# Optimization experiments

Measured on AMD Instinct MI355X. Metric: run time of the kernel, lower is better.

Reference implementation:

```python
import jax, jax.numpy as jnp
import numpy as np

EMBED_DIM = 1024
NUM_HEADS = 16
HEAD_DIM = EMBED_DIM // NUM_HEADS  # 64
GROUP_SIZE = 4                     # 4 values packed per uint8 (2-bit KIVI)
Q_LEVELS = 3.0                     # 2-bit -> codes in [0, 3]
Q_HALF = 1.5                       # symmetric offset


def kivi_fake_quant(k):
    """Per-group 2-bit quantize+dequantize of keys, KIVI-style.
    k: [B, H, S, D] float32. Groups of GROUP_SIZE along D share one fp32 scale
    (mirrors k_cache_packed uint8 codes + k_scales fp32 in the source).
    """
    B, H, S, D = k.shape
    g = k.reshape(B, H, S, D // GROUP_SIZE, GROUP_SIZE)
    max_abs = jnp.max(jnp.abs(g), axis=-1, keepdims=True)        # per-group scale basis
    scale = max_abs / Q_HALF
    safe = jnp.where(scale == 0, 1.0, scale)
    codes = jnp.clip(jnp.round(g / safe + Q_HALF), 0.0, Q_LEVELS)  # uint8 codes (as float)
    deq = (codes - Q_HALF) * scale                                 # dequant
    return deq.reshape(B, H, S, D)


def split_heads(x):
    B, S, E = x.shape
    return x.reshape(B, S, NUM_HEADS, HEAD_DIM).transpose(0, 2, 1, 3)  # [B,H,S,d]


def setup_inputs() -> dict:
    key = jax.random.key(0)
    k1, k2, k3 = jax.random.split(key, 3)
    B, S = 4, 1024
    return {
        "hidden_states": jax.random.normal(k1, (B, S, EMBED_DIM), jnp.float32),
        "attention_mask": jnp.zeros((B, S), jnp.float32),  # additive mask
        "w_attn": jax.random.normal(k2, (EMBED_DIM, 3 * EMBED_DIM), jnp.float32) * 0.02,
        "b_attn": jnp.zeros((3 * EMBED_DIM,), jnp.float32),
        "w_proj": jax.random.normal(k3, (EMBED_DIM, EMBED_DIM), jnp.float32) * 0.02,
        "b_proj": jnp.zeros((EMBED_DIM,), jnp.float32),
    }


def reference(hidden_states, attention_mask, w_attn, b_attn, w_proj, b_proj):
    B, S, E = hidden_states.shape
    qkv = hidden_states @ w_attn + b_attn            # GPT-2 Conv1D: x @ W + b
    q, k, v = jnp.split(qkv, 3, axis=2)
    q, k, v = split_heads(q), split_heads(k), split_heads(v)   # [B,H,S,d]

    k_deq = kivi_fake_quant(k)                       # quantized KV cache (keys)
    # kivi_sycl.batched_attention: q @ dequant(K)^T over full cache_len (== S here)
    scores = jnp.einsum('bhqd,bhkd->bhqk', q, k_deq)
    # source adds 2-D additive mask BEFORE the 1/sqrt(d) scaling
    scores = scores + attention_mask[:, None, None, :]
    attn = jax.nn.softmax(scores / jnp.sqrt(jnp.float32(HEAD_DIM)), axis=-1)

    out = jnp.einsum('bhqk,bhkd->bhqd', attn, v)     # V cache kept fp32
    out = out.transpose(0, 2, 1, 3).reshape(B, S, E)
    return out @ w_proj + b_proj
```

## Files before the change

### kernel.cpp

```cpp
#include <hip/hip_runtime.h>
#include <math.h>

#define S_LEN 1024
#define B_SZ  4
#define E_DIM 1024
#define NH    16
#define HD    64
#define GK    1024

typedef unsigned short u16;
typedef _Float16 f16;
typedef __attribute__((ext_vector_type(8))) _Float16 f16x8;
typedef __attribute__((ext_vector_type(2))) __fp16   hf16x2;
typedef __attribute__((ext_vector_type(4))) float    f32x4;

#define MFMA16(a, b, c) __builtin_amdgcn_mfma_f32_16x16x32_f16(a, b, c, 0, 0, 0)
#define SCALE2 0.18033688011112042f

__device__ __forceinline__ u16 f2h_bits(float f) {
    union { f16 h; u16 u; } c; c.h = (f16)f;
    return c.u;
}
__device__ __forceinline__ unsigned pk2h(float a, float b) {
    return (unsigned)f2h_bits(a) | ((unsigned)f2h_bits(b) << 16);
}
__device__ __forceinline__ unsigned pkrtz2(float a, float b) {
    hf16x2 t = __builtin_amdgcn_cvt_pkrtz(a, b);
    union { hf16x2 v; unsigned u; } c; c.v = t; return c.u;
}

__device__ __forceinline__ void glds16(const u16* g, u16* l) {
    __builtin_amdgcn_global_load_lds(
        (const __attribute__((address_space(1))) unsigned int*)g,
        (__attribute__((address_space(3))) unsigned int*)l, 16, 0, 0);
}

__global__ __launch_bounds__(256) void prep_all(
    const float* __restrict__ hs, u16* __restrict__ Hh,
    const float* __restrict__ w_attn, u16* __restrict__ Wqt,
    const float* __restrict__ w_proj, u16* __restrict__ Wpt,
    const float* __restrict__ mask, float* __restrict__ Msc)
{
    __shared__ float t[32][33];
    const int bid = blockIdx.x;

    if (bid == 8192) {
        const int i = threadIdx.x * 16;
        #pragma unroll
        for (int k = 0; k < 4; ++k) {
            float4 v = *(const float4*)&mask[i + 4 * k];
            float4 o = { v.x * SCALE2, v.y * SCALE2, v.z * SCALE2, v.w * SCALE2 };
            *(float4*)&Msc[i + 4 * k] = o;
        }
        return;
    }
    if (bid < 4096) {
        const size_t i = ((size_t)bid * 256 + threadIdx.x) * 4;
        float4 v = *(const float4*)&hs[i];
        ushort4 h;
        h.x = f2h_bits(v.x); h.y = f2h_bits(v.y);
        h.z = f2h_bits(v.z); h.w = f2h_bits(v.w);
        *(ushort4*)&Hh[i] = h;
        return;
    }

    const bool isA = bid < 7168;
    const int tt = isA ? (bid - 4096) : (bid - 7168);
    const int bxx = isA ? (tt % 96) : (tt % 32);
    const int byy = isA ? (tt / 96) : (tt / 32);
    const int N   = isA ? 3072 : 1024;
    const float* W = isA ? w_attn : w_proj;
    u16* Wt = isA ? Wqt : Wpt;

    const int k0 = byy * 32, n0 = bxx * 32;
    {
        const int kr = threadIdx.x >> 3, nc = (threadIdx.x & 7) << 2;
        float4 v = *(const float4*)&W[(size_t)(k0 + kr) * N + n0 + nc];
        t[kr][nc] = v.x; t[kr][nc + 1] = v.y; t[kr][nc + 2] = v.z; t[kr][nc + 3] = v.w;
    }
    __syncthreads();
    const int nr = threadIdx.x >> 3, kc = (threadIdx.x & 7) << 2;
    ushort4 h;
    h.x = f2h_bits(t[kc + 0][nr]); h.y = f2h_bits(t[kc + 1][nr]);
    h.z = f2h_bits(t[kc + 2][nr]); h.w = f2h_bits(t[kc + 3][nr]);
    *(ushort4*)&Wt[(size_t)(n0 + nr) * GK + k0 + kc] = h;
}

__global__ __launch_bounds__(256, 3) void qkv_gemm(
    const u16* __restrict__ A, const u16* __restrict__ Bt,
    const float* __restrict__ bias, u16* __restrict__ Qh,
    u16* __restrict__ Kh, u16* __restrict__ Vtg)
{
    __shared__ u16 SLDS[16896];
    u16* Asp = SLDS;
    u16* Bsp = SLDS + 8192;

    const int tid = threadIdx.x;
    const int wave = tid >> 6, lane = tid & 63;
    const int quad = lane >> 4, l15 = lane & 15;
    const int wr = wave >> 1, wc = wave & 1;

    const int m0   = blockIdx.y * 128;
    const int nloc = blockIdx.x * 128;
    const int region = nloc >> 10;

    const u16* Ab = A  + (size_t)m0 * GK;
    const u16* Bb = Bt + (size_t)nloc * GK;

    const int soff = (((lane & 7) ^ ((lane >> 3) & 7)) << 3);
    const int srow8 = lane >> 3;
    const int sw = l15 & 7;

    f32x4 acc[4][4] = {};

    for (int k0 = 0; k0 < GK; k0 += 64) {
        __syncthreads();
        #pragma unroll
        for (int i = 0; i < 4; ++i) {
            const int tI = wave * 4 + i;
            const int row = tI * 8 + srow8;
            glds16(Ab + (size_t)row * GK + k0 + soff, &Asp[tI * 512]);
            glds16(Bb + (size_t)row * GK + k0 + soff, &Bsp[tI * 512]);
        }
        __syncthreads();
        #pragma unroll
        for (int h = 0; h < 2; ++h) {
            const int cs = ((4 * h + quad) ^ sw) << 3;
            f16x8 af[4], bf[4];
            #pragma unroll
            for (int i = 0; i < 4; ++i)
                af[i] = *(const f16x8*)&Asp[(64 * wr + 16 * i + l15) * 64 + cs];
            #pragma unroll
            for (int j = 0; j < 4; ++j)
                bf[j] = *(const f16x8*)&Bsp[(64 * wc + 16 * j + l15) * 64 + cs];
            #pragma unroll
            for (int i = 0; i < 4; ++i)
                #pragma unroll
                for (int j = 0; j < 4; ++j)
                    acc[i][j] = MFMA16(af[i], bf[j], acc[i][j]);
        }
    }

    if (region == 2) {
        #pragma unroll
        for (int j = 0; j < 4; ++j) {
            const int colg = nloc + 64 * wc + 16 * j + l15;
            const float bv = bias[colg];
            const int cr = colg & 1023, h = cr >> 6, d = cr & 63;
            #pragma unroll
            for (int i = 0; i < 4; ++i) {
                const int rowb = m0 + 64 * wr + 16 * i + quad * 4;
                const int b = rowb >> 10, s0 = rowb & 1023;
                float v0 = acc[i][j][0] + bv, v1 = acc[i][j][1] + bv;
                float v2 = acc[i][j][2] + bv, v3 = acc[i][j][3] + bv;
                uint2 st = { pk2h(v0, v1), pk2h(v2, v3) };
                *(uint2*)&Vtg[((size_t)(b * NH + h) * HD + d) * S_LEN + s0] = st;
            }
        }
    } else {
        float* EP = (float*)SLDS;
        u16* dstg = (region == 1) ? Kh : Qh;
        #pragma unroll
        for (int p = 0; p < 2; ++p) {
            __syncthreads();
            if (wr == p) {
                #pragma unroll
                for (int i = 0; i < 4; ++i)
                    #pragma unroll
                    for (int j = 0; j < 4; ++j) {
                        const int colb = 64 * wc + 16 * j + l15;
                        const float bv = bias[nloc + colb];
                        #pragma unroll
                        for (int r = 0; r < 4; ++r)
                            EP[(16 * i + quad * 4 + r) * 132 + colb] = acc[i][j][r] + bv;
                    }
            }
            __syncthreads();
            const int rr = tid >> 2, cc = (tid & 3) * 32;
            const int rowg = m0 + 64 * p + rr;
            const int bb = rowg >> 10, ss = rowg & 1023;
            float v[32];
            #pragma unroll
            for (int k = 0; k < 8; ++k) {
                f32x4 t4 = *(const f32x4*)&EP[rr * 132 + cc + 4 * k];
                v[4 * k + 0] = t4[0]; v[4 * k + 1] = t4[1];
                v[4 * k + 2] = t4[2]; v[4 * k + 3] = t4[3];
            }
            if (region == 1) {
                #pragma unroll
                for (int g = 0; g < 8; ++g) {
                    float a = fmaxf(fmaxf(fabsf(v[4 * g]), fabsf(v[4 * g + 1])),
                                    fmaxf(fabsf(v[4 * g + 2]), fabsf(v[4 * g + 3])));
                    float scale = a * (1.0f / 1.5f);
                    float safe  = (scale == 0.0f) ? 1.0f : scale;
                    #pragma unroll
                    for (int r = 0; r < 4; ++r) {
                        float q = fminf(fmaxf(rintf(v[4 * g + r] / safe + 1.5f), 0.0f), 3.0f);
                        v[4 * g + r] = (q - 1.5f) * scale;
                    }
                }
            }
            unsigned w[16];
            #pragma unroll
            for (int m = 0; m < 16; ++m) w[m] = pk2h(v[2 * m], v[2 * m + 1]);
            const int hh = ((nloc & 1023) + cc) >> 6;
            const int d0 = cc & 63;
            u16* dp = dstg + (((size_t)(bb * NH + hh)) * S_LEN + ss) * HD + d0;
            #pragma unroll
            for (int q4 = 0; q4 < 4; ++q4) {
                uint4 st = { w[4 * q4], w[4 * q4 + 1], w[4 * q4 + 2], w[4 * q4 + 3] };
                *(uint4*)&dp[q4 * 8] = st;
            }
        }
    }
}

__global__ __launch_bounds__(256, 4) void proj_gemm(
    const u16* __restrict__ A, const u16* __restrict__ Bt,
    const float* __restrict__ bias, float* __restrict__ C)
{
    __shared__ u16 Asp[64 * 64];
    __shared__ u16 Bsp[128 * 64];

    const int tid = threadIdx.x;
    const int wave = tid >> 6, lane = tid & 63;
    const int quad = lane >> 4, l15 = lane & 15;
    const int wr = wave >> 1, wc = wave & 1;

    const int m0   = blockIdx.y * 64;
    const int nloc = blockIdx.x * 128;

    const u16* Ab = A  + (size_t)m0 * GK;
    const u16* Bb = Bt + (size_t)nloc * GK;

    const int soff = (((lane & 7) ^ ((lane >> 3) & 7)) << 3);
    const int srow8 = lane >> 3;
    const int sw = l15 & 7;

    f32x4 acc[2][4] = {};

    for (int k0 = 0; k0 < GK; k0 += 64) {
        __syncthreads();
        #pragma unroll
        for (int i = 0; i < 2; ++i) {
            const int tI = wave * 2 + i;
            glds16(Ab + (size_t)(tI * 8 + srow8) * GK + k0 + soff, &Asp[tI * 512]);
        }
        #pragma unroll
        for (int i = 0; i < 4; ++i) {
            const int tI = wave * 4 + i;
            glds16(Bb + (size_t)(tI * 8 + srow8) * GK + k0 + soff, &Bsp[tI * 512]);
        }
        __syncthreads();
        #pragma unroll
        for (int h = 0; h < 2; ++h) {
            const int cs = ((4 * h + quad) ^ sw) << 3;
            f16x8 af[2], bf[4];
            #pragma unroll
            for (int i = 0; i < 2; ++i)
                af[i] = *(const f16x8*)&Asp[(32 * wr + 16 * i + l15) * 64 + cs];
            #pragma unroll
            for (int j = 0; j < 4; ++j)
                bf[j] = *(const f16x8*)&Bsp[(64 * wc + 16 * j + l15) * 64 + cs];
            #pragma unroll
            for (int i = 0; i < 2; ++i)
                #pragma unroll
                for (int j = 0; j < 4; ++j)
                    acc[i][j] = MFMA16(af[i], bf[j], acc[i][j]);
        }
    }

    #pragma unroll
    for (int j = 0; j < 4; ++j) {
        const int col = nloc + 64 * wc + 16 * j + l15;
        const float bv = bias[col];
        #pragma unroll
        for (int i = 0; i < 2; ++i) {
            const int row = m0 + 32 * wr + 16 * i + quad * 4;
            #pragma unroll
            for (int r = 0; r < 4; ++r)
                C[(size_t)(row + r) * E_DIM + col] = acc[i][j][r] + bv;
        }
    }
}

__global__ __launch_bounds__(256) void attn_mfma(
    const u16* __restrict__ Qh, const u16* __restrict__ Kh,
    const u16* __restrict__ Vtg, const float* __restrict__ Msc,
    u16* __restrict__ out)
{
    __shared__ u16 KsL[64 * 64];
    __shared__ u16 VtL[64 * 64];
    __shared__ u16 Ps[4][16 * 72];

    const int tid  = threadIdx.x;
    const int wave = tid >> 6, lane = tid & 63;
    const int quad = lane >> 4, l15 = lane & 15;

    const int blk = blockIdx.x;
    const int qt = blk & 15;
    const int h  = (blk >> 4) & 15;
    const int b  = blk >> 8;
    const size_t head_base = (size_t)(b * NH + h) * (S_LEN * HD);

    const int qbase = qt * 64 + wave * 16;
    f16x8 qf0, qf1;
    {
        const u16* qp = Qh + head_base + (size_t)(qbase + l15) * HD + quad * 8;
        qf0 = *(const f16x8*)qp;
        qf1 = *(const f16x8*)(qp + 32);
    }

    f32x4 O[4] = {};
    f32x4 ps_acc = {0.f, 0.f, 0.f, 0.f};

    const int srow_ = wave * 8 + (lane >> 3);
    const int skoff = (((lane & 7) ^ ((lane >> 3) & 7)) << 3);
    const int ch0 = (((0 + quad) ^ (l15 & 7)) << 3);
    const int ch1 = (((4 + quad) ^ (l15 & 7)) << 3);

    for (int kt = 0; kt < 16; ++kt) {
        __syncthreads();
        #pragma unroll
        for (int p = 0; p < 2; ++p) {
            const int srow = p * 32 + srow_;
            glds16(Kh  + head_base + (size_t)(kt * 64 + srow) * HD + skoff,
                   &KsL[p * 2048 + wave * 512]);
            glds16(Vtg + head_base + (size_t)srow * S_LEN + kt * 64 + skoff,
                   &VtL[p * 2048 + wave * 512]);
        }
        __syncthreads();

        f32x4 acc[4] = {};
        #pragma unroll
        for (int i = 0; i < 4; ++i) {
            const u16* kr = &KsL[(16 * i + l15) * 64];
            acc[i] = MFMA16(*(const f16x8*)&kr[ch0], qf0, acc[i]);
            acc[i] = MFMA16(*(const f16x8*)&kr[ch1], qf1, acc[i]);
        }

        const float* mrow = Msc + b * S_LEN + kt * 64;
        f32x4 p4[4];
        #pragma unroll
        for (int i = 0; i < 4; ++i) {
            f32x4 mk = *(const f32x4*)(mrow + 16 * i + quad * 4);
            f32x4 s = acc[i] * SCALE2 + mk;
            p4[i][0] = __builtin_amdgcn_exp2f(s[0]);
            p4[i][1] = __builtin_amdgcn_exp2f(s[1]);
            p4[i][2] = __builtin_amdgcn_exp2f(s[2]);
            p4[i][3] = __builtin_amdgcn_exp2f(s[3]);
            ps_acc += p4[i];
        }

        {
            u16* pw = &Ps[wave][l15 * 72];
            #pragma unroll
            for (int i = 0; i < 4; ++i) {
                *(unsigned*)&pw[16 * i + quad * 4]     = pkrtz2(p4[i][0], p4[i][1]);
                *(unsigned*)&pw[16 * i + quad * 4 + 2] = pkrtz2(p4[i][2], p4[i][3]);
            }
        }

        #pragma unroll
        for (int kc = 0; kc < 2; ++kc) {
            f16x8 pa = *(const f16x8*)&Ps[wave][l15 * 72 + kc * 32 + quad * 8];
            const int chv = kc ? ch1 : ch0;
            #pragma unroll
            for (int i = 0; i < 4; ++i)
                O[i] = MFMA16(pa, *(const f16x8*)&VtL[(16 * i + l15) * 64 + chv], O[i]);
        }
    }

    float psum = (ps_acc[0] + ps_acc[1]) + (ps_acc[2] + ps_acc[3]);
    psum += __shfl_xor(psum, 16);
    psum += __shfl_xor(psum, 32);
    float li[4];
    #pragma unroll
    for (int r = 0; r < 4; ++r) li[r] = 1.0f / __shfl(psum, quad * 4 + r);
    #pragma unroll
    for (int r = 0; r < 4; ++r) {
        u16* orow = out + ((size_t)(b * S_LEN) + qbase + quad * 4 + r) * E_DIM
                    + h * HD + l15;
        orow[0]  = f2h_bits(O[0][r] * li[r]);
        orow[16] = f2h_bits(O[1][r] * li[r]);
        orow[32] = f2h_bits(O[2][r] * li[r]);
        orow[48] = f2h_bits(O[3][r] * li[r]);
    }
}

extern "C" void kernel_launch(void* const* d_in, const int* in_sizes, int n_in,
                              void* d_out, int out_size, void* d_ws, size_t ws_size,
                              hipStream_t stream)
{
    const float* hs     = (const float*)d_in[0];
    const float* mask   = (const float*)d_in[1];
    const float* w_attn = (const float*)d_in[2];
    const float* b_attn = (const float*)d_in[3];
    const float* w_proj = (const float*)d_in[4];
    const float* b_proj = (const float*)d_in[5];
    float* out = (float*)d_out;

    const size_t M1 = (size_t)4096 * 1024;
    u16* Ah   = (u16*)d_ws;
    u16* Wqt  = Ah   + M1;
    u16* Wpt  = Wqt  + 3 * M1;
    u16* Qh   = Wpt  + M1;
    u16* Kh   = Qh   + M1;
    u16* Vtg  = Kh   + M1;
    u16* AOh  = Vtg  + M1;
    float* Msc = (float*)(AOh + M1);

    prep_all<<<8193, 256, 0, stream>>>(hs, Ah, w_attn, Wqt, w_proj, Wpt, mask, Msc);

    qkv_gemm<<<dim3(24, 32), 256, 0, stream>>>(Ah, Wqt, b_attn, Qh, Kh, Vtg);

    attn_mfma<<<B_SZ * NH * (S_LEN / 64), 256, 0, stream>>>(Qh, Kh, Vtg, Msc, AOh);

    proj_gemm<<<dim3(8, 64), 256, 0, stream>>>(AOh, Wpt, b_proj, out);
}
```

Baseline: 171.4 us.

## Load K/V fragments directly from global into registers, drop LDS staging

The attention kernel no longer stages K and V tiles through shared memory with block-wide barriers. Each wave now loads its own MFMA operand fragments straight from global memory (relying on L2/L1 reuse across the four waves). It also remaps block indices so blocks sharing a head are scheduled together, sets launch bounds to target 4 blocks per CU, and raises wave priority around the MFMA sections. This removes the LDS traffic and __syncthreads, but each wave now issues redundant global loads and the loads are no longer overlapped with compute through a shared stage.

```diff
diff --git a/kernel.cpp b/kernel.cpp
--- a/kernel.cpp
+++ b/kernel.cpp
@@ -284,24 +284,22 @@
     }
 }
 
-__global__ __launch_bounds__(256) void attn_mfma(
+__global__ __launch_bounds__(256, 4) void attn_mfma(
     const u16* __restrict__ Qh, const u16* __restrict__ Kh,
     const u16* __restrict__ Vtg, const float* __restrict__ Msc,
     u16* __restrict__ out)
 {
-    __shared__ u16 KsL[64 * 64];
-    __shared__ u16 VtL[64 * 64];
     __shared__ u16 Ps[4][16 * 72];
 
     const int tid  = threadIdx.x;
     const int wave = tid >> 6, lane = tid & 63;
     const int quad = lane >> 4, l15 = lane & 15;
 
-    const int blk = blockIdx.x;
-    const int qt = blk & 15;
-    const int h  = (blk >> 4) & 15;
-    const int b  = blk >> 8;
-    const size_t head_base = (size_t)(b * NH + h) * (S_LEN * HD);
+    const int d = blockIdx.x;
+    const int head = (d & 7) * 8 + (d >> 7);
+    const int qt   = (d >> 3) & 15;
+    const int b = head >> 4, h = head & 15;
+    const size_t head_base = (size_t)head * (S_LEN * HD);
 
     const int qbase = qt * 64 + wave * 16;
     f16x8 qf0, qf1;
@@ -314,29 +312,32 @@
     f32x4 O[4] = {};
     f32x4 ps_acc = {0.f, 0.f, 0.f, 0.f};
 
-    const int srow_ = wave * 8 + (lane >> 3);
-    const int skoff = (((lane & 7) ^ ((lane >> 3) & 7)) << 3);
-    const int ch0 = (((0 + quad) ^ (l15 & 7)) << 3);
-    const int ch1 = (((4 + quad) ^ (l15 & 7)) << 3);
+    const u16* Kb = Kh  + head_base;
+    const u16* Vb = Vtg + head_base;
 
     for (int kt = 0; kt < 16; ++kt) {
-        __syncthreads();
-        #pragma unroll
-        for (int p = 0; p < 2; ++p) {
-            const int srow = p * 32 + srow_;
-            glds16(Kh  + head_base + (size_t)(kt * 64 + srow) * HD + skoff,
-                   &KsL[p * 2048 + wave * 512]);
-            glds16(Vtg + head_base + (size_t)srow * S_LEN + kt * 64 + skoff,
-                   &VtL[p * 2048 + wave * 512]);
-        }
-        __syncthreads();
-
+        f16x8 ka[4], kb2[4];
+        #pragma unroll
+        for (int i = 0; i < 4; ++i) {
+            const u16* kr = Kb + (size_t)(kt * 64 + 16 * i + l15) * HD + quad * 8;
+            ka[i]  = *(const f16x8*)kr;
+            kb2[i] = *(const f16x8*)(kr + 32);
+        }
         f32x4 acc[4] = {};
-        #pragma unroll
-        for (int i = 0; i < 4; ++i) {
-            const u16* kr = &KsL[(16 * i + l15) * 64];
-            acc[i] = MFMA16(*(const f16x8*)&kr[ch0], qf0, acc[i]);
-            acc[i] = MFMA16(*(const f16x8*)&kr[ch1], qf1, acc[i]);
+        __builtin_amdgcn_s_setprio(1);
+        #pragma unroll
+        for (int i = 0; i < 4; ++i) {
+            acc[i] = MFMA16(ka[i],  qf0, acc[i]);
+            acc[i] = MFMA16(kb2[i], qf1, acc[i]);
+        }
+        __builtin_amdgcn_s_setprio(0);
+
+        f16x8 va[4], vb2[4];
+        #pragma unroll
+        for (int i = 0; i < 4; ++i) {
+            const u16* vr = Vb + (size_t)(16 * i + l15) * S_LEN + kt * 64 + quad * 8;
+            va[i]  = *(const f16x8*)vr;
+            vb2[i] = *(const f16x8*)(vr + 32);
         }
 
         const float* mrow = Msc + b * S_LEN + kt * 64;
@@ -361,14 +362,15 @@
             }
         }
 
+        __builtin_amdgcn_s_setprio(1);
         #pragma unroll
         for (int kc = 0; kc < 2; ++kc) {
             f16x8 pa = *(const f16x8*)&Ps[wave][l15 * 72 + kc * 32 + quad * 8];
-            const int chv = kc ? ch1 : ch0;
             #pragma unroll
             for (int i = 0; i < 4; ++i)
-                O[i] = MFMA16(pa, *(const f16x8*)&VtL[(16 * i + l15) * 64 + chv], O[i]);
-        }
+                O[i] = MFMA16(pa, kc ? vb2[i] : va[i], O[i]);
+        }
+        __builtin_amdgcn_s_setprio(0);
     }
 
     float psum = (ps_acc[0] + ps_acc[1]) + (ps_acc[2] + ps_acc[3]);
```

New measurement: 258.5 us. 1.51x slower.
